# Kernel optimization log

Measured on AMD Instinct MI355X. Metric: run time of the kernel, lower is better.

The kernel has to match this reference:

```python
import jax, jax.numpy as jnp
import numpy as np
from jax import lax

CLIP = 10.0


def setup_inputs() -> dict:
    key = jax.random.key(0)
    k1, k2, k3, k4 = jax.random.split(key, 4)
    B, T, I, H = 64, 512, 512, 512
    x = jax.random.normal(k1, (B, T, I), dtype=jnp.float32)
    kernel = jax.random.normal(k2, (I, H), dtype=jnp.float32) * 0.05
    recurrent_kernel = jax.random.normal(k3, (H, H), dtype=jnp.float32) * 0.05
    bias_i = jax.random.normal(k4, (H,), dtype=jnp.float32) * 0.05
    h0 = jnp.zeros((B, H), dtype=jnp.float32)
    return {"x": x, "kernel": kernel, "recurrent_kernel": recurrent_kernel,
            "bias_i": bias_i, "h0": h0}


def reference(x, kernel, recurrent_kernel, bias_i, h0):
    # Elman RNN: Ht = tanh(clip(Xt@W + Ht-1@R + b, -clip, clip))
    def step(h, xt):
        g = xt @ kernel + h @ recurrent_kernel + bias_i  # [B, H]
        h_new = jnp.tanh(jnp.clip(g, -CLIP, CLIP))
        return h_new, h_new

    xs = jnp.swapaxes(x, 0, 1)  # [T, B, I] for scan over time
    h_last, ys = lax.scan(step, h0, xs)
    outputs = jnp.swapaxes(ys, 0, 1)  # [B, T, H]
    return outputs, h_last
```

## Files before the change

kernel.cpp:

```cpp
#include <hip/hip_runtime.h>

#define Bdim 64
#define Tdim 512
#define Idim 512
#define Hdim 512
#define CLIPV 10.0f
#define NREGG 50
#define NLDSG 14

typedef __attribute__((ext_vector_type(4))) float f32x4;
typedef __attribute__((ext_vector_type(8))) short bf16x8;
typedef _Float16 half2v __attribute__((ext_vector_type(2)));

__device__ __forceinline__ ushort f2bf(float f) {
    unsigned u = __builtin_bit_cast(unsigned, f);
    u += 0x7fffu + ((u >> 16) & 1u);
    return (ushort)(u >> 16);
}
__device__ __forceinline__ float bf2f(ushort h) {
    return __builtin_bit_cast(float, (unsigned)h << 16);
}
__device__ __forceinline__ void split_bf(float f, ushort& h, ushort& l) {
    h = f2bf(f);
    l = f2bf(f - bf2f(h));
}
__device__ __forceinline__ float dot2acc(uint r, uint h2, float acc) {
#if __has_builtin(__builtin_amdgcn_fdot2)
    return __builtin_amdgcn_fdot2(__builtin_bit_cast(half2v, r),
                                  __builtin_bit_cast(half2v, h2), acc, false);
#else
    half2v a = __builtin_bit_cast(half2v, r);
    half2v b = __builtin_bit_cast(half2v, h2);
    return acc + (float)a.x * (float)b.x + (float)a.y * (float)b.y;
#endif
}
__device__ __forceinline__ uint packf16(float a, float b) {
    _Float16 fa = (_Float16)a, fb = (_Float16)b;
    return (uint)__builtin_bit_cast(ushort, fa) |
           ((uint)__builtin_bit_cast(ushort, fb) << 16);
}
__device__ __forceinline__ ushort f2h(float f) {
    _Float16 h = (_Float16)f;
    return __builtin_bit_cast(ushort, h);
}
__device__ __forceinline__ float fastrcp(float x) {
#if __has_builtin(__builtin_amdgcn_rcpf)
    return __builtin_amdgcn_rcpf(x);
#else
    return 1.0f / x;
#endif
}

__global__ __launch_bounds__(256) void transpose_w_kernel(const float* __restrict__ w,
                                                          ushort* __restrict__ wth,
                                                          ushort* __restrict__ wtl) {
    int idx = blockIdx.x * 256 + threadIdx.x;
    int k = idx >> 9, n = idx & 511;
    ushort h, l;
    split_bf(w[idx], h, l);
    wth[n * Idim + k] = h;
    wtl[n * Idim + k] = l;
}

__global__ __launch_bounds__(256) void pack_r_kernel(const float* __restrict__ Rw,
                                                     uint* __restrict__ rpk) {
    int d = blockIdx.x * 256 + threadIdx.x;
    int g = d >> 11;
    int rem = d & 2047;
    int t = rem >> 2, r = rem & 3;
    int j = g >> 1, half = g & 1;
    int kp = (t >> 6) * 32 + j;
    int c  = (t & 63) * 8 + half * 4 + r;
    rpk[d] = packf16(Rw[(size_t)(2 * kp) * Hdim + c],
                     Rw[(size_t)(2 * kp + 1) * Hdim + c]);
}

#define BM 128
#define BN 128
#define BK 32
__global__ __launch_bounds__(256) void gemm_xw(
    const float* __restrict__ A,
    const ushort* __restrict__ Bth,
    const ushort* __restrict__ Btl,
    const float* __restrict__ bias,
    float* __restrict__ C,
    int M, int N, int K)
{
    __shared__ ushort AsH[BM][BK];
    __shared__ ushort AsL[BM][BK];
    __shared__ ushort BsH[BN][BK];
    __shared__ ushort BsL[BN][BK];
    int bm = blockIdx.x, bn = blockIdx.y;
    int tid = threadIdx.x;
    int wave = tid >> 6, lane = tid & 63;
    int wr = wave >> 1, wc = wave & 1;
    f32x4 acc[4][4] = {};
    const int row0 = bm * BM, col0 = bn * BN;
    const int sr = tid >> 1;
    const int sc = (tid & 1) * 16;

    for (int kt = 0; kt < K; kt += BK) {
        const float* gA = A + (size_t)(row0 + sr) * K + kt + sc;
        #pragma unroll
        for (int q = 0; q < 4; ++q) {
            float4 v = *(const float4*)(gA + q * 4);
            ushort4 h4, l4;
            split_bf(v.x, h4.x, l4.x);
            split_bf(v.y, h4.y, l4.y);
            split_bf(v.z, h4.z, l4.z);
            split_bf(v.w, h4.w, l4.w);
            *(ushort4*)&AsH[sr][sc + q * 4] = h4;
            *(ushort4*)&AsL[sr][sc + q * 4] = l4;
        }
        const int4* gBh = (const int4*)(Bth + (size_t)(col0 + sr) * K + kt + sc);
        *(int4*)&BsH[sr][sc]     = gBh[0];
        *(int4*)&BsH[sr][sc + 8] = gBh[1];
        const int4* gBl = (const int4*)(Btl + (size_t)(col0 + sr) * K + kt + sc);
        *(int4*)&BsL[sr][sc]     = gBl[0];
        *(int4*)&BsL[sr][sc + 8] = gBl[1];
        __syncthreads();

        const int r = lane & 15, kg = lane >> 4;
        bf16x8 ah[4], al[4], bh[4], bl[4];
        #pragma unroll
        for (int m = 0; m < 4; ++m) {
            ah[m] = *(const bf16x8*)&AsH[wr * 64 + m * 16 + r][kg * 8];
            al[m] = *(const bf16x8*)&AsL[wr * 64 + m * 16 + r][kg * 8];
        }
        #pragma unroll
        for (int n = 0; n < 4; ++n) {
            bh[n] = *(const bf16x8*)&BsH[wc * 64 + n * 16 + r][kg * 8];
            bl[n] = *(const bf16x8*)&BsL[wc * 64 + n * 16 + r][kg * 8];
        }
        #pragma unroll
        for (int m = 0; m < 4; ++m)
            #pragma unroll
            for (int n = 0; n < 4; ++n) {
                acc[m][n] = __builtin_amdgcn_mfma_f32_16x16x32_bf16(ah[m], bh[n], acc[m][n], 0, 0, 0);
                acc[m][n] = __builtin_amdgcn_mfma_f32_16x16x32_bf16(ah[m], bl[n], acc[m][n], 0, 0, 0);
                acc[m][n] = __builtin_amdgcn_mfma_f32_16x16x32_bf16(al[m], bh[n], acc[m][n], 0, 0, 0);
            }
        __syncthreads();
    }

    const int cl = lane & 15, rg = lane >> 4;
    #pragma unroll
    for (int n = 0; n < 4; ++n) {
        int gc = col0 + wc * 64 + n * 16 + cl;
        float bv = bias[gc];
        #pragma unroll
        for (int m = 0; m < 4; ++m) {
            int gr = row0 + wr * 64 + m * 16 + rg * 4;
            #pragma unroll
            for (int r2 = 0; r2 < 4; ++r2)
                C[(size_t)(gr + r2) * N + gc] = acc[m][n][r2] + bv;
        }
    }
}

__global__ __launch_bounds__(512, 2) void rnn_reg_kernel(
    const uint* __restrict__ Rpk,
    float* __restrict__ out,
    float* __restrict__ hlast,
    const float* __restrict__ h0)
{
    __shared__ uint Rlds[NLDSG * 2048];
    __shared__ ushort h1[Hdim];
    __shared__ float part[2][8][Hdim];

    const int tid = threadIdx.x;
    const int row = blockIdx.x;
    const int w   = tid >> 6;
    const int l   = tid & 63;
    const int col = w * 64 + l;

    uint4 rr4[NREGG];
    const uint* rbase = Rpk + tid * 4;
    #pragma unroll
    for (int i = 0; i < NREGG; ++i)
        rr4[i] = *(const uint4*)(rbase + i * 2048);
    #pragma unroll
    for (int g = 0; g < NLDSG; ++g)
        *(uint4*)&Rlds[g * 2048 + tid * 4] =
            *(const uint4*)(rbase + (NREGG + g) * 2048);

    h1[tid] = f2h(h0[row * Hdim + tid]);
    __syncthreads();

    float* orow = out + (size_t)row * Tdim * Hdim;

    for (int t = 0; t < Tdim; ++t, orow += Hdim) {
        float pre = orow[col];
        uint hval = ((const uint*)h1)[w * 32 + (l & 31)];

        float a0 = 0.f, a1 = 0.f, a2 = 0.f, a3 = 0.f;
        float a4 = 0.f, a5 = 0.f, a6 = 0.f, a7 = 0.f;
        #pragma unroll
        for (int j = 0; j < NREGG / 2; ++j) {
            uint hvi = __builtin_amdgcn_readlane(hval, j);
            uint4 rA = rr4[2 * j], rB = rr4[2 * j + 1];
            a0 = dot2acc(rA.x, hvi, a0);
            a1 = dot2acc(rA.y, hvi, a1);
            a2 = dot2acc(rA.z, hvi, a2);
            a3 = dot2acc(rA.w, hvi, a3);
            a4 = dot2acc(rB.x, hvi, a4);
            a5 = dot2acc(rB.y, hvi, a5);
            a6 = dot2acc(rB.z, hvi, a6);
            a7 = dot2acc(rB.w, hvi, a7);
        }
        #pragma unroll
        for (int j = 0; j < NLDSG / 2; ++j) {
            uint hvi = __builtin_amdgcn_readlane(hval, NREGG / 2 + j);
            uint4 rA = *(const uint4*)&Rlds[(2 * j) * 2048 + tid * 4];
            uint4 rB = *(const uint4*)&Rlds[(2 * j + 1) * 2048 + tid * 4];
            a0 = dot2acc(rA.x, hvi, a0);
            a1 = dot2acc(rA.y, hvi, a1);
            a2 = dot2acc(rA.z, hvi, a2);
            a3 = dot2acc(rA.w, hvi, a3);
            a4 = dot2acc(rB.x, hvi, a4);
            a5 = dot2acc(rB.y, hvi, a5);
            a6 = dot2acc(rB.z, hvi, a6);
            a7 = dot2acc(rB.w, hvi, a7);
        }
        const int p = t & 1;
        *(f32x4*)&part[p][w][l * 8]     = (f32x4){a0, a1, a2, a3};
        *(f32x4*)&part[p][w][l * 8 + 4] = (f32x4){a4, a5, a6, a7};
        __syncthreads();

        float s = pre;
        #pragma unroll
        for (int e = 0; e < 8; ++e) s += part[p][e][col];
        s = fminf(fmaxf(s, -CLIPV), CLIPV);
        float e2 = __expf(2.0f * s);
        float v = (e2 - 1.0f) * fastrcp(e2 + 1.0f);
        orow[col] = v;
        h1[col] = f2h(v);
        if (t == Tdim - 1) hlast[row * Hdim + col] = v;
    }
}

extern "C" void kernel_launch(void* const* d_in, const int* in_sizes, int n_in,
                              void* d_out, int out_size, void* d_ws, size_t ws_size,
                              hipStream_t stream) {
    const float* x    = (const float*)d_in[0];
    const float* W    = (const float*)d_in[1];
    const float* R    = (const float*)d_in[2];
    const float* bias = (const float*)d_in[3];
    const float* h0   = (const float*)d_in[4];
    float* out = (float*)d_out;

    ushort* wth = (ushort*)d_ws;
    ushort* wtl = wth + (size_t)Idim * Hdim;
    uint* rpk   = (uint*)((char*)d_ws + (1u << 20));

    transpose_w_kernel<<<(Idim * Hdim + 255) / 256, 256, 0, stream>>>(W, wth, wtl);
    pack_r_kernel<<<512, 256, 0, stream>>>(R, rpk);

    dim3 gg(Bdim * Tdim / BM, Hdim / BN);
    gemm_xw<<<gg, 256, 0, stream>>>(x, wth, wtl, bias, out, Bdim * Tdim, Hdim, Idim);

    rnn_reg_kernel<<<Bdim, 512, 0, stream>>>(
        rpk, out, out + (size_t)Bdim * Tdim * Hdim, h0);
}
```

Before: 780.9 us.

## Keep recurrent hidden state in registers and prefetch next-step preactivations

The shared-memory h1 broadcast buffer is removed. Each wave now reduces the partial sums for its own 64-wide k-slice, two columns per lane, and packs the new hidden values into a register with cvt_pkrtz for the next step's readlane. The recurrent-weight packing layout is remapped so columns match this ownership. The next step's input preactivation is loaded one step ahead to hide global latency. The aim is to cut the LDS round trip and latency on the serial critical path, at the cost of half the lanes doing duplicate tanh work, round-toward-zero fp16 rounding, and a prefetch that reads past the current row on the last step.

```diff
diff --git a/kernel.cpp b/kernel.cpp
--- a/kernel.cpp
+++ b/kernel.cpp
@@ -11,6 +11,7 @@
 typedef __attribute__((ext_vector_type(4))) float f32x4;
 typedef __attribute__((ext_vector_type(8))) short bf16x8;
 typedef _Float16 half2v __attribute__((ext_vector_type(2)));
+typedef __fp16 fp16x2 __attribute__((ext_vector_type(2)));
 
 __device__ __forceinline__ ushort f2bf(float f) {
     unsigned u = __builtin_bit_cast(unsigned, f);
@@ -39,9 +40,13 @@
     return (uint)__builtin_bit_cast(ushort, fa) |
            ((uint)__builtin_bit_cast(ushort, fb) << 16);
 }
-__device__ __forceinline__ ushort f2h(float f) {
-    _Float16 h = (_Float16)f;
-    return __builtin_bit_cast(ushort, h);
+__device__ __forceinline__ uint pkrtz(float a, float b) {
+#if __has_builtin(__builtin_amdgcn_cvt_pkrtz)
+    fp16x2 p = __builtin_amdgcn_cvt_pkrtz(a, b);
+    return __builtin_bit_cast(uint, p);
+#else
+    return packf16(a, b);
+#endif
 }
 __device__ __forceinline__ float fastrcp(float x) {
 #if __has_builtin(__builtin_amdgcn_rcpf)
@@ -69,8 +74,9 @@
     int rem = d & 2047;
     int t = rem >> 2, r = rem & 3;
     int j = g >> 1, half = g & 1;
-    int kp = (t >> 6) * 32 + j;
-    int c  = (t & 63) * 8 + half * 4 + r;
+    int w = t >> 6, l = t & 63;
+    int kp = w * 32 + j;
+    int c  = half * 256 + l * 4 + r;
     rpk[d] = packf16(Rw[(size_t)(2 * kp) * Hdim + c],
                      Rw[(size_t)(2 * kp + 1) * Hdim + c]);
 }
@@ -165,14 +171,14 @@
     const float* __restrict__ h0)
 {
     __shared__ uint Rlds[NLDSG * 2048];
-    __shared__ ushort h1[Hdim];
     __shared__ float part[2][8][Hdim];
 
     const int tid = threadIdx.x;
     const int row = blockIdx.x;
     const int w   = tid >> 6;
     const int l   = tid & 63;
-    const int col = w * 64 + l;
+    const int li  = l & 31;
+    const int fcol = w * 64 + 2 * li;
 
     uint4 rr4[NREGG];
     const uint* rbase = Rpk + tid * 4;
@@ -184,14 +190,14 @@
         *(uint4*)&Rlds[g * 2048 + tid * 4] =
             *(const uint4*)(rbase + (NREGG + g) * 2048);
 
-    h1[tid] = f2h(h0[row * Hdim + tid]);
+    uint hval = packf16(h0[row * Hdim + fcol], h0[row * Hdim + fcol + 1]);
     __syncthreads();
 
     float* orow = out + (size_t)row * Tdim * Hdim;
+    float2 pre = *(const float2*)(orow + fcol);
 
     for (int t = 0; t < Tdim; ++t, orow += Hdim) {
-        float pre = orow[col];
-        uint hval = ((const uint*)h1)[w * 32 + (l & 31)];
+        float2 pre_nxt = *(const float2*)(orow + Hdim + fcol);
 
         float a0 = 0.f, a1 = 0.f, a2 = 0.f, a3 = 0.f;
         float a4 = 0.f, a5 = 0.f, a6 = 0.f, a7 = 0.f;
@@ -223,19 +229,28 @@
             a7 = dot2acc(rB.w, hvi, a7);
         }
         const int p = t & 1;
-        *(f32x4*)&part[p][w][l * 8]     = (f32x4){a0, a1, a2, a3};
-        *(f32x4*)&part[p][w][l * 8 + 4] = (f32x4){a4, a5, a6, a7};
+        *(f32x4*)&part[p][w][l * 4]       = (f32x4){a0, a1, a2, a3};
+        *(f32x4*)&part[p][w][256 + l * 4] = (f32x4){a4, a5, a6, a7};
         __syncthreads();
 
-        float s = pre;
-        #pragma unroll
-        for (int e = 0; e < 8; ++e) s += part[p][e][col];
-        s = fminf(fmaxf(s, -CLIPV), CLIPV);
-        float e2 = __expf(2.0f * s);
-        float v = (e2 - 1.0f) * fastrcp(e2 + 1.0f);
-        orow[col] = v;
-        h1[col] = f2h(v);
-        if (t == Tdim - 1) hlast[row * Hdim + col] = v;
+        float s0 = pre.x, s1 = pre.y;
+        #pragma unroll
+        for (int e = 0; e < 8; ++e) {
+            float2 pp = *(const float2*)&part[p][e][fcol];
+            s0 += pp.x; s1 += pp.y;
+        }
+        s0 = fminf(fmaxf(s0, -CLIPV), CLIPV);
+        s1 = fminf(fmaxf(s1, -CLIPV), CLIPV);
+        float e0 = __expf(2.0f * s0), e1 = __expf(2.0f * s1);
+        float v0 = (e0 - 1.0f) * fastrcp(e0 + 1.0f);
+        float v1 = (e1 - 1.0f) * fastrcp(e1 + 1.0f);
+        hval = pkrtz(v0, v1);
+        if (l < 32) {
+            *(float2*)(orow + fcol) = make_float2(v0, v1);
+            if (t == Tdim - 1)
+                *(float2*)&hlast[row * Hdim + fcol] = make_float2(v0, v1);
+        }
+        pre = pre_nxt;
     }
 }
 
```

Result: slower. 844.6 us (+8.2%).

## Compute recurrent h@R step with f16 MFMA instead of per-lane fdot2

Applied to the files above, without the earlier changes.

The recurrent matvec now uses 16x16x32 f16 MFMA instructions. Each wave covers 64 output columns over the full K dimension, taking the hidden state as a broadcast A operand and holding R fragments in registers plus LDS. This removes the cross-wave partial-sum buffer and the 8-way reduction after the barrier. The hidden state is double-buffered in LDS, and the next step's precomputed input projection is prefetched. Only one row of each MFMA output is used, so most of the matrix-core work is wasted.

```diff
diff --git a/kernel.cpp b/kernel.cpp
--- a/kernel.cpp
+++ b/kernel.cpp
@@ -5,12 +5,12 @@
 #define Idim 512
 #define Hdim 512
 #define CLIPV 10.0f
-#define NREGG 50
-#define NLDSG 14
+#define NREGKT 12
+#define NLDSKT 4
 
 typedef __attribute__((ext_vector_type(4))) float f32x4;
 typedef __attribute__((ext_vector_type(8))) short bf16x8;
-typedef _Float16 half2v __attribute__((ext_vector_type(2)));
+typedef _Float16 f16x8 __attribute__((ext_vector_type(8)));
 
 __device__ __forceinline__ ushort f2bf(float f) {
     unsigned u = __builtin_bit_cast(unsigned, f);
@@ -23,16 +23,6 @@
 __device__ __forceinline__ void split_bf(float f, ushort& h, ushort& l) {
     h = f2bf(f);
     l = f2bf(f - bf2f(h));
-}
-__device__ __forceinline__ float dot2acc(uint r, uint h2, float acc) {
-#if __has_builtin(__builtin_amdgcn_fdot2)
-    return __builtin_amdgcn_fdot2(__builtin_bit_cast(half2v, r),
-                                  __builtin_bit_cast(half2v, h2), acc, false);
-#else
-    half2v a = __builtin_bit_cast(half2v, r);
-    half2v b = __builtin_bit_cast(half2v, h2);
-    return acc + (float)a.x * (float)b.x + (float)a.y * (float)b.y;
-#endif
 }
 __device__ __forceinline__ uint packf16(float a, float b) {
     _Float16 fa = (_Float16)a, fb = (_Float16)b;
@@ -65,14 +55,14 @@
 __global__ __launch_bounds__(256) void pack_r_kernel(const float* __restrict__ Rw,
                                                      uint* __restrict__ rpk) {
     int d = blockIdx.x * 256 + threadIdx.x;
-    int g = d >> 11;
-    int rem = d & 2047;
-    int t = rem >> 2, r = rem & 3;
-    int j = g >> 1, half = g & 1;
-    int kp = (t >> 6) * 32 + j;
-    int c  = (t & 63) * 8 + half * 4 + r;
-    rpk[d] = packf16(Rw[(size_t)(2 * kp) * Hdim + c],
-                     Rw[(size_t)(2 * kp + 1) * Hdim + c]);
+    int g = d >> 8;
+    int kt = g >> 5, C = g & 31;
+    int rem = d & 255;
+    int l = rem >> 2, q = rem & 3;
+    int col = C * 16 + (l & 15);
+    int k = kt * 32 + (l >> 4) * 8 + 2 * q;
+    rpk[d] = packf16(Rw[(size_t)k * Hdim + col],
+                     Rw[(size_t)(k + 1) * Hdim + col]);
 }
 
 #define BM 128
@@ -158,84 +148,98 @@
     }
 }
 
-__global__ __launch_bounds__(512, 2) void rnn_reg_kernel(
+__global__ __launch_bounds__(512, 2) void rnn_mfma_kernel(
     const uint* __restrict__ Rpk,
     float* __restrict__ out,
     float* __restrict__ hlast,
     const float* __restrict__ h0)
 {
-    __shared__ uint Rlds[NLDSG * 2048];
-    __shared__ ushort h1[Hdim];
-    __shared__ float part[2][8][Hdim];
+    __shared__ uint Rlds[NLDSKT * 4 * 2048];
+    __shared__ ushort h16[2][Hdim];
 
     const int tid = threadIdx.x;
     const int row = blockIdx.x;
     const int w   = tid >> 6;
     const int l   = tid & 63;
-    const int col = w * 64 + l;
-
-    uint4 rr4[NREGG];
-    const uint* rbase = Rpk + tid * 4;
-    #pragma unroll
-    for (int i = 0; i < NREGG; ++i)
-        rr4[i] = *(const uint4*)(rbase + i * 2048);
-    #pragma unroll
-    for (int g = 0; g < NLDSG; ++g)
-        *(uint4*)&Rlds[g * 2048 + tid * 4] =
-            *(const uint4*)(rbase + (NREGG + g) * 2048);
-
-    h1[tid] = f2h(h0[row * Hdim + tid]);
+    const int lr  = l & 15;
+    const int kg  = l >> 4;
+
+    uint4 breg[NREGKT][4];
+    const uint* rb = Rpk + l * 4;
+    #pragma unroll
+    for (int kt = 0; kt < NREGKT; ++kt)
+        #pragma unroll
+        for (int c = 0; c < 4; ++c)
+            breg[kt][c] = *(const uint4*)(rb + (kt * 32 + w * 4 + c) * 256);
+    #pragma unroll
+    for (int kt = 0; kt < NLDSKT; ++kt)
+        #pragma unroll
+        for (int c = 0; c < 4; ++c)
+            *(uint4*)&Rlds[(kt * 4 + c) * 2048 + tid * 4] =
+                *(const uint4*)(rb + ((NREGKT + kt) * 32 + w * 4 + c) * 256);
+
+    h16[0][tid] = f2h(h0[row * Hdim + tid]);
     __syncthreads();
 
     float* orow = out + (size_t)row * Tdim * Hdim;
+    float pre[4];
+    #pragma unroll
+    for (int c = 0; c < 4; ++c)
+        pre[c] = orow[w * 64 + c * 16 + lr];
 
     for (int t = 0; t < Tdim; ++t, orow += Hdim) {
-        float pre = orow[col];
-        uint hval = ((const uint*)h1)[w * 32 + (l & 31)];
-
-        float a0 = 0.f, a1 = 0.f, a2 = 0.f, a3 = 0.f;
-        float a4 = 0.f, a5 = 0.f, a6 = 0.f, a7 = 0.f;
-        #pragma unroll
-        for (int j = 0; j < NREGG / 2; ++j) {
-            uint hvi = __builtin_amdgcn_readlane(hval, j);
-            uint4 rA = rr4[2 * j], rB = rr4[2 * j + 1];
-            a0 = dot2acc(rA.x, hvi, a0);
-            a1 = dot2acc(rA.y, hvi, a1);
-            a2 = dot2acc(rA.z, hvi, a2);
-            a3 = dot2acc(rA.w, hvi, a3);
-            a4 = dot2acc(rB.x, hvi, a4);
-            a5 = dot2acc(rB.y, hvi, a5);
-            a6 = dot2acc(rB.z, hvi, a6);
-            a7 = dot2acc(rB.w, hvi, a7);
-        }
-        #pragma unroll
-        for (int j = 0; j < NLDSG / 2; ++j) {
-            uint hvi = __builtin_amdgcn_readlane(hval, NREGG / 2 + j);
-            uint4 rA = *(const uint4*)&Rlds[(2 * j) * 2048 + tid * 4];
-            uint4 rB = *(const uint4*)&Rlds[(2 * j + 1) * 2048 + tid * 4];
-            a0 = dot2acc(rA.x, hvi, a0);
-            a1 = dot2acc(rA.y, hvi, a1);
-            a2 = dot2acc(rA.z, hvi, a2);
-            a3 = dot2acc(rA.w, hvi, a3);
-            a4 = dot2acc(rB.x, hvi, a4);
-            a5 = dot2acc(rB.y, hvi, a5);
-            a6 = dot2acc(rB.z, hvi, a6);
-            a7 = dot2acc(rB.w, hvi, a7);
-        }
         const int p = t & 1;
-        *(f32x4*)&part[p][w][l * 8]     = (f32x4){a0, a1, a2, a3};
-        *(f32x4*)&part[p][w][l * 8 + 4] = (f32x4){a4, a5, a6, a7};
+        float pren[4];
+        #pragma unroll
+        for (int c = 0; c < 4; ++c)
+            pren[c] = orow[Hdim + w * 64 + c * 16 + lr];
+
+        f32x4 acc0 = {}, acc1 = {}, acc2 = {}, acc3 = {};
+        #pragma unroll
+        for (int kt = 0; kt < 16; ++kt) {
+            f16x8 a = *(const f16x8*)&h16[p][kt * 32 + kg * 8];
+            if (kt < NREGKT) {
+                acc0 = __builtin_amdgcn_mfma_f32_16x16x32_f16(
+                    a, __builtin_bit_cast(f16x8, breg[kt][0]), acc0, 0, 0, 0);
+                acc1 = __builtin_amdgcn_mfma_f32_16x16x32_f16(
+                    a, __builtin_bit_cast(f16x8, breg[kt][1]), acc1, 0, 0, 0);
+                acc2 = __builtin_amdgcn_mfma_f32_16x16x32_f16(
+                    a, __builtin_bit_cast(f16x8, breg[kt][2]), acc2, 0, 0, 0);
+                acc3 = __builtin_amdgcn_mfma_f32_16x16x32_f16(
+                    a, __builtin_bit_cast(f16x8, breg[kt][3]), acc3, 0, 0, 0);
+            } else {
+                uint4 b0 = *(const uint4*)&Rlds[((kt - NREGKT) * 4 + 0) * 2048 + tid * 4];
+                uint4 b1 = *(const uint4*)&Rlds[((kt - NREGKT) * 4 + 1) * 2048 + tid * 4];
+                uint4 b2 = *(const uint4*)&Rlds[((kt - NREGKT) * 4 + 2) * 2048 + tid * 4];
+                uint4 b3 = *(const uint4*)&Rlds[((kt - NREGKT) * 4 + 3) * 2048 + tid * 4];
+                acc0 = __builtin_amdgcn_mfma_f32_16x16x32_f16(
+                    a, __builtin_bit_cast(f16x8, b0), acc0, 0, 0, 0);
+                acc1 = __builtin_amdgcn_mfma_f32_16x16x32_f16(
+                    a, __builtin_bit_cast(f16x8, b1), acc1, 0, 0, 0);
+                acc2 = __builtin_amdgcn_mfma_f32_16x16x32_f16(
+                    a, __builtin_bit_cast(f16x8, b2), acc2, 0, 0, 0);
+                acc3 = __builtin_amdgcn_mfma_f32_16x16x32_f16(
+                    a, __builtin_bit_cast(f16x8, b3), acc3, 0, 0, 0);
+            }
+        }
+
+        if (l < 16) {
+            float s[4] = {acc0[0], acc1[0], acc2[0], acc3[0]};
+            #pragma unroll
+            for (int c = 0; c < 4; ++c) {
+                float g = s[c] + pre[c];
+                g = fminf(fmaxf(g, -CLIPV), CLIPV);
+                float e = __expf(2.0f * g);
+                float v = (e - 1.0f) * fastrcp(e + 1.0f);
+                int col = w * 64 + c * 16 + l;
+                h16[p ^ 1][col] = f2h(v);
+                orow[col] = v;
+                if (t == Tdim - 1) hlast[row * Hdim + col] = v;
+            }
+        }
         __syncthreads();
-
-        float s = pre;
-        #pragma unroll
-        for (int e = 0; e < 8; ++e) s += part[p][e][col];
-        s = fminf(fmaxf(s, -CLIPV), CLIPV);
-        float e2 = __expf(2.0f * s);
-        float v = (e2 - 1.0f) * fastrcp(e2 + 1.0f);
-        orow[col] = v;
-        h1[col] = f2h(v);
-        if (t == Tdim - 1) hlast[row * Hdim + col] = v;
+        #pragma unroll
+        for (int c = 0; c < 4; ++c) pre[c] = pren[c];
     }
 }
 
@@ -259,6 +263,6 @@
     dim3 gg(Bdim * Tdim / BM, Hdim / BN);
     gemm_xw<<<gg, 256, 0, stream>>>(x, wth, wtl, bias, out, Bdim * Tdim, Hdim, Idim);
 
-    rnn_reg_kernel<<<Bdim, 512, 0, stream>>>(
+    rnn_mfma_kernel<<<Bdim, 512, 0, stream>>>(
         rpk, out, out + (size_t)Bdim * Tdim * Hdim, h0);
 }
```

Measured after the change: 786.6 us. Within noise of the previous version (+0.7%).
